# Performance work log

Measured on AMD Instinct MI355X. Metric: run time of the kernel, lower is better.

The kernel has to match this reference:

```python
import jax, jax.numpy as jnp
import numpy as np

T, B, E, H = 2048, 2, 1024, 16
DH = E // H
SCALE = DH ** -0.5
NEG = jnp.finfo(jnp.float32).min


def setup_inputs() -> dict:
    key = jax.random.key(0)
    ks = jax.random.split(key, 10)
    s = 0.02
    query = jax.random.normal(ks[0], (T, B, E), dtype=jnp.float32)
    key_padding_mask = jax.random.randint(ks[1], (B, T), 0, 2).astype(bool)
    # causal additive mask, broadcastable over (bsz, heads, tgt, src)
    causal = jnp.triu(jnp.ones((T, T), dtype=bool), k=1)
    attn_mask = jnp.where(causal, NEG, 0.0).astype(jnp.float32)[None, None]
    Wq = jax.random.normal(ks[2], (E, E), jnp.float32) * s
    bq = jax.random.normal(ks[3], (E,), jnp.float32) * s
    Wk = jax.random.normal(ks[4], (E, E), jnp.float32) * s
    bk = jax.random.normal(ks[5], (E,), jnp.float32) * s
    Wv = jax.random.normal(ks[6], (E, E), jnp.float32) * s
    bv = jax.random.normal(ks[7], (E,), jnp.float32) * s
    Wo = jax.random.normal(ks[8], (E, E), jnp.float32) * s
    bo = jax.random.normal(ks[9], (E,), jnp.float32) * s
    return {"query": query, "key_padding_mask": key_padding_mask, "attn_mask": attn_mask,
            "Wq": Wq, "bq": bq, "Wk": Wk, "bk": bk, "Wv": Wv, "bv": bv, "Wo": Wo, "bo": bo}


def _heads(x):
    # [T, B, E] -> [B, H, T, DH]
    return x.reshape(T, B, H, DH).transpose(1, 2, 0, 3)


def reference(query, key_padding_mask, attn_mask, Wq, bq, Wk, bk, Wv, bv, Wo, bo):
    # projections (torch Linear: x @ W.T + b); q scaled as in module
    q = _heads((query @ Wq.T + bq) * SCALE)          # [B,H,T,DH]
    k = _heads(query @ Wk.T + bk)                    # [B,H,S,DH] (self-attn: S=T)
    v = _heads(query @ Wv.T + bv)
    scores = jnp.einsum('bhtd,bhsd->bhts', q, k)     # [B,H,T,S]
    scores = scores + attn_mask                      # additive causal mask
    # key_padding_mask True -> masked_fill with dtype min
    scores = jnp.where(key_padding_mask[:, None, None, :], NEG, scores)
    probs = jax.nn.softmax(scores, axis=-1)
    ctx = jnp.einsum('bhts,bhsd->bhtd', probs, v)    # [B,H,T,DH]
    ctx = ctx.transpose(2, 0, 1, 3).reshape(T, B, E) # back to [T,B,E]
    return ctx @ Wo.T + bo
```

## Files before the change

### kernel.cpp

```cpp
#include <hip/hip_runtime.h>
#include <hip/hip_bf16.h>
#include <stdint.h>

typedef unsigned short u16;
typedef uint32_t u32;
typedef unsigned long long u64;
typedef __attribute__((ext_vector_type(8))) short bf16x8;
typedef __attribute__((ext_vector_type(4))) float f32x4;
typedef __attribute__((ext_vector_type(16))) float f32x16;
typedef __attribute__((ext_vector_type(4))) u32 u32x4;

#define T_SEQ 2048

__device__ __forceinline__ float bf2f(u16 u) {
  union { u32 i; float f; } v; v.i = ((u32)u) << 16; return v.f;
}
__device__ __forceinline__ u16 f2bf(float f) {
  union { float f; u32 i; } v; v.f = f;
  u32 u = v.i;
  return (u16)((u + 0x7fffu + ((u >> 16) & 1u)) >> 16);
}

#if __has_builtin(__builtin_amdgcn_exp2f)
#define EXP2F(x) __builtin_amdgcn_exp2f(x)
#else
#define EXP2F(x) exp2f(x)
#endif

__device__ __forceinline__ u32 permpack(float lo, float hi) {
#if __has_builtin(__builtin_amdgcn_perm)
  return __builtin_amdgcn_perm(__float_as_uint(hi), __float_as_uint(lo), 0x07060302u);
#else
  return (__float_as_uint(hi) & 0xFFFF0000u) | (__float_as_uint(lo) >> 16);
#endif
}

__device__ __forceinline__ void gload_lds16(const void* g, void* l) {
  __builtin_amdgcn_global_load_lds(
      (const __attribute__((address_space(1))) void*)g,
      (__attribute__((address_space(3))) void*)l, 16, 0, 0);
}

__global__ __launch_bounds__(256) void cvt_kernel(const float* __restrict__ src,
                                                  u16* __restrict__ dst, int n) {
  int i = (blockIdx.x * 256 + threadIdx.x) * 4;
  if (i + 3 < n) {
    const float4 v = *(const float4*)(src + i);
    ushort4 o;
    o.x = f2bf(v.x); o.y = f2bf(v.y); o.z = f2bf(v.z); o.w = f2bf(v.w);
    *(ushort4*)(dst + i) = o;
  }
}

__global__ __launch_bounds__(256) void cvt4_kernel(
    const float* __restrict__ s0, const float* __restrict__ s1,
    const float* __restrict__ s2, const float* __restrict__ s3,
    u16* __restrict__ dst) {
  const int z = blockIdx.y;
  const float* src = (z == 0) ? s0 : (z == 1) ? s1 : (z == 2) ? s2 : s3;
  int i = (blockIdx.x * 256 + threadIdx.x) * 4;
  const float4 v = *(const float4*)(src + i);
  ushort4 o;
  o.x = f2bf(v.x); o.y = f2bf(v.y); o.z = f2bf(v.z); o.w = f2bf(v.w);
  *(ushort4*)(dst + (size_t)z * 1048576 + i) = o;
}

__device__ __forceinline__ void gemm_core_128x128(
    f32x4 acc[2][4], const u16* __restrict__ A, const u16* __restrict__ Bw,
    int bm, int bn, u16* As, u16* Bs)
{
  const int tid = threadIdx.x;
  const int w = tid >> 6, lane = tid & 63, g = lane >> 4, c = lane & 15;
  const int wr = (w & 3) * 32, wc = (w >> 2) * 64;
  for (int k0 = 0; k0 < 1024; k0 += 64) {
    __syncthreads();
    #pragma unroll
    for (int is = 0; is < 2; ++is) {
      int o = (is*8 + w)*1024 + lane*16;
      int row = o >> 7, c16 = (o >> 4) & 7;
      gload_lds16(A + (size_t)(bm*128 + row)*1024 + k0 + (c16 ^ (row & 7))*8,
                  (char*)As + (is*8 + w)*1024);
    }
    #pragma unroll
    for (int is = 0; is < 2; ++is) {
      int o = (is*8 + w)*1024 + lane*16;
      int row = o >> 7, c16 = (o >> 4) & 7;
      gload_lds16(Bw + (size_t)(bn*128 + row)*1024 + k0 + (c16 ^ (row & 7))*8,
                  (char*)Bs + (is*8 + w)*1024);
    }
    __syncthreads();
    bf16x8 af[2][2], bfr[4][2];
    #pragma unroll
    for (int mf = 0; mf < 2; ++mf)
      #pragma unroll
      for (int kc = 0; kc < 2; ++kc) {
        int row = wr + mf*16 + c;
        int colb = kc*64 + g*16;
        af[mf][kc] = *(const bf16x8*)((const char*)As + row*128 + (colb ^ ((row & 7) << 4)));
      }
    #pragma unroll
    for (int nf = 0; nf < 4; ++nf)
      #pragma unroll
      for (int kc = 0; kc < 2; ++kc) {
        int row = wc + nf*16 + c;
        int colb = kc*64 + g*16;
        bfr[nf][kc] = *(const bf16x8*)((const char*)Bs + row*128 + (colb ^ ((row & 7) << 4)));
      }
    #pragma unroll
    for (int mf = 0; mf < 2; ++mf)
      #pragma unroll
      for (int nf = 0; nf < 4; ++nf)
        #pragma unroll
        for (int kc = 0; kc < 2; ++kc)
          acc[mf][nf] = __builtin_amdgcn_mfma_f32_16x16x32_bf16(
              af[mf][kc], bfr[nf][kc], acc[mf][nf], 0, 0, 0);
  }
}

__global__ __launch_bounds__(512, 2) void gemm_qkv(
    const u16* __restrict__ Abf, const u16* __restrict__ Wbf,
    const float* __restrict__ bq, const float* __restrict__ bk,
    const float* __restrict__ bv, u16* __restrict__ qkvh)
{
  __shared__ __align__(16) u16 As[128*64];
  __shared__ __align__(16) u16 Bs[128*64];
  f32x4 acc[2][4];
  #pragma unroll
  for (int mf = 0; mf < 2; ++mf)
    #pragma unroll
    for (int nf = 0; nf < 4; ++nf) acc[mf][nf] = (f32x4){0.f,0.f,0.f,0.f};
  gemm_core_128x128(acc, Abf, Wbf, blockIdx.x, blockIdx.y, As, Bs);
  const int tid = threadIdx.x, w = tid >> 6, lane = tid & 63, g = lane >> 4, c = lane & 15;
  const int wr = (w & 3) * 32, wc = (w >> 2) * 64;
  #pragma unroll
  for (int mf = 0; mf < 2; ++mf)
    #pragma unroll
    for (int nf = 0; nf < 4; ++nf) {
      int col = blockIdx.y*128 + wc + nf*16 + c;
      int z = col >> 10, colz = col & 1023;
      const float* bias = (z == 0) ? bq : (z == 1) ? bk : bv;
      float bcol = bias[colz];
      float scl = (z == 0) ? 0.18033688011112043f : 1.0f;
      int h = colz >> 6, d = colz & 63;
      u16* dst = qkvh + (size_t)z * 4194304;
      #pragma unroll
      for (int r = 0; r < 4; ++r) {
        int row = blockIdx.x*128 + wr + mf*16 + g*4 + r;
        int t = row >> 1, bb = row & 1;
        float v = (acc[mf][nf][r] + bcol) * scl;
        dst[(size_t)(bb*16 + h)*131072 + (size_t)t*64 + d] = f2bf(v);
      }
    }
}

__global__ __launch_bounds__(512, 2) void gemm_out(
    const u16* __restrict__ ctx2, const u16* __restrict__ Wobf,
    const float* __restrict__ bo, float* __restrict__ out)
{
  __shared__ __align__(16) u16 As[128*64];
  __shared__ __align__(16) u16 Bs[128*64];
  f32x4 acc[2][4];
  #pragma unroll
  for (int mf = 0; mf < 2; ++mf)
    #pragma unroll
    for (int nf = 0; nf < 4; ++nf) acc[mf][nf] = (f32x4){0.f,0.f,0.f,0.f};
  gemm_core_128x128(acc, ctx2, Wobf, blockIdx.x, blockIdx.y, As, Bs);
  const int tid = threadIdx.x, w = tid >> 6, lane = tid & 63, g = lane >> 4, c = lane & 15;
  const int wr = (w & 3) * 32, wc = (w >> 2) * 64;
  #pragma unroll
  for (int mf = 0; mf < 2; ++mf)
    #pragma unroll
    for (int nf = 0; nf < 4; ++nf) {
      int col = blockIdx.y*128 + wc + nf*16 + c;
      float bcol = bo[col];
      #pragma unroll
      for (int r = 0; r < 4; ++r) {
        int row = blockIdx.x*128 + wr + mf*16 + g*4 + r;
        out[(size_t)row*1024 + col] = acc[mf][nf][r] + bcol;
      }
    }
}

__global__ __launch_bounds__(256) void vtrans_kernel(const u16* __restrict__ Vh,
                                                     u16* __restrict__ Vt,
                                                     float* __restrict__ vs) {
  __shared__ u16 tile[64][72];
  const int bh = blockIdx.x >> 5, tc = blockIdx.x & 31;
  const int t0 = tc * 64;
  const int tid = threadIdx.x;
  {
    const int tl = tid >> 2, d0 = (tid & 3) * 16;
    const u16* src = Vh + (size_t)bh*131072 + (size_t)(t0 + tl)*64 + d0;
    bf16x8 a = *(const bf16x8*)src;
    bf16x8 b2 = *(const bf16x8*)(src + 8);
    #pragma unroll
    for (int j = 0; j < 8; ++j) {
      tile[d0 + j][tl] = (u16)a[j];
      tile[d0 + 8 + j][tl] = (u16)b2[j];
    }
  }
  __syncthreads();
  {
    const int d = tid >> 2, tq = (tid & 3) * 16;
    bf16x8 o0, o1;
    float s = 0.f;
    #pragma unroll
    for (int j = 0; j < 8; ++j) {
      u16 x0 = tile[d][tq + j], x1 = tile[d][tq + 8 + j];
      o0[j] = (short)x0; o1[j] = (short)x1;
      s += bf2f(x0) + bf2f(x1);
    }
    u16* dst = Vt + (size_t)bh*131072 + (size_t)d*2048 + t0 + tq;
    *(bf16x8*)dst = o0;
    *(bf16x8*)(dst + 8) = o1;
    s += __shfl_xor(s, 1, 64);
    s += __shfl_xor(s, 2, 64);
    if ((tid & 3) == 0) atomicAdd(&vs[bh*64 + d], s);
  }
}

#define ZERO16 (f32x16){0.f,0.f,0.f,0.f,0.f,0.f,0.f,0.f,0.f,0.f,0.f,0.f,0.f,0.f,0.f,0.f}
#define NEGINF (-__builtin_inff())

__global__ __launch_bounds__(128, 2) void flash_attn(
    const u16* __restrict__ Qh, const u16* __restrict__ Kh,
    const u16* __restrict__ Vt, const int* __restrict__ kpm,
    const float* __restrict__ vsum, u16* __restrict__ ctx2,
    u16* __restrict__ pctx, float* __restrict__ pml)
{
  __shared__ __align__(16) u16 Kl[2][4096];
  __shared__ __align__(16) u16 Vl[2][4096];

  const int tid = threadIdx.x;
  const int w = tid >> 6, lane = tid & 63;
  const int l31 = lane & 31, hi = lane >> 5;

  const int id = blockIdx.x;
  const int xcd = id & 7, rest = id >> 3;
  const int bh = xcd * 4 + (rest & 3);
  const int pr = rest >> 2;
  int k, ch, NS;
  if (pr < 32) { k = 31 - (pr >> 1); ch = pr & 1; NS = 2; }
  else         { k = 47 - pr;        ch = 0;      NS = 1; }
  const int nt = k + 1;
  const int b = bh >> 4, h = bh & 15;
  const size_t hbase = (size_t)bh * 131072;
  int lo, hicap;
  if (NS == 1) { lo = 0; hicap = nt; }
  else { int h1 = nt >> 1; lo = ch ? h1 : 0; hicap = ch ? nt : h1; }
  const int q = k*64 + w*32 + l31;

  bf16x8 qfrag[4];
  #pragma unroll
  for (int kt = 0; kt < 4; ++kt)
    qfrag[kt] = *(const bf16x8*)(Qh + hbase + (size_t)q*64 + kt*16 + hi*8);

  {
    const int s0t = lo * 64;
    if (w == 0) {
      #pragma unroll
      for (int is = 0; is < 8; ++is) {
        int o = is*1024 + lane*16;
        int row = o >> 7, c16 = (o >> 4) & 7;
        gload_lds16(Kh + hbase + (size_t)(s0t + row)*64 + (c16 ^ (row & 7))*8,
                    (char*)Kl[0] + is*1024);
      }
    } else {
      #pragma unroll
      for (int is = 0; is < 8; ++is) {
        int o = is*1024 + lane*16;
        int row = o >> 7, c16 = (o >> 4) & 7;
        gload_lds16(Vt + hbase + (size_t)row*2048 + s0t + (c16 ^ (row & 7))*8,
                    (char*)Vl[0] + is*1024);
      }
    }
  }
  int kpmv_cur = kpm[b*T_SEQ + lo*64 + lane];
  int kpmv_nxt = 0;
  __syncthreads();

  float mrow = NEGINF, lrow = 0.f;
  f32x16 cacc0 = ZERO16, cacc1 = ZERO16;

  for (int t = lo; t < hicap; ++t) {
    const int cur = (t - lo) & 1, nxt = cur ^ 1;
    const int s0 = t * 64;
    const bool notLast = (t + 1 < hicap);
    const bool diag = (t == nt - 1);

    if (notLast) {
      const int s0n = s0 + 64;
      if (w == 0) {
        #pragma unroll
        for (int is = 0; is < 8; ++is) {
          int o = is*1024 + lane*16;
          int row = o >> 7, c16 = (o >> 4) & 7;
          gload_lds16(Kh + hbase + (size_t)(s0n + row)*64 + (c16 ^ (row & 7))*8,
                      (char*)Kl[nxt] + is*1024);
        }
      } else {
        #pragma unroll
        for (int is = 0; is < 8; ++is) {
          int o = is*1024 + lane*16;
          int row = o >> 7, c16 = (o >> 4) & 7;
          gload_lds16(Vt + hbase + (size_t)row*2048 + s0n + (c16 ^ (row & 7))*8,
                      (char*)Vl[nxt] + is*1024);
        }
      }
      kpmv_nxt = kpm[b*T_SEQ + s0n + lane];
    }

    bf16x8 kreg[2][4], vf[2][4];
    #pragma unroll
    for (int sub = 0; sub < 2; ++sub)
      #pragma unroll
      for (int kt = 0; kt < 4; ++kt) {
        int row = sub*32 + l31;
        int colb = kt*32 + hi*16;
        kreg[sub][kt] = *(const bf16x8*)((const char*)Kl[cur] + row*128 + (colb ^ ((row & 7) << 4)));
        vf[sub][kt]   = *(const bf16x8*)((const char*)Vl[cur] + row*128 + (colb ^ ((row & 7) << 4)));
      }

    f32x16 st0 = ZERO16, st1 = ZERO16;
    __builtin_amdgcn_s_setprio(1);
    #pragma unroll
    for (int kt = 0; kt < 4; ++kt) {
      st0 = __builtin_amdgcn_mfma_f32_32x32x16_bf16(kreg[0][kt], qfrag[kt], st0, 0, 0, 0);
      st1 = __builtin_amdgcn_mfma_f32_32x32x16_bf16(kreg[1][kt], qfrag[kt], st1, 0, 0, 0);
    }
    __builtin_amdgcn_s_setprio(0);

    {
      const u64 mask = __ballot(kpmv_cur != 0);
      const u32 m0 = (u32)mask, m1 = (u32)(mask >> 32);
      const u64 m4 = mask >> 4;
      const u32 m4l = (u32)m4, m4h = (u32)(m4 >> 32);
      const u32 w0 = hi ? m4l : m0;
      const u32 w1 = hi ? m4h : m1;
      const int lim = q - s0 - 4*hi;
      #pragma unroll
      for (int m = 0; m < 4; ++m) {
        u32 nib0 = (w0 >> (m*8)) & 15u;
        u32 nib1 = (w1 >> (m*8)) & 15u;
        if (diag) {
          int t0c = lim - m*8;       int c0 = min(max(t0c + 1, 0), 4);
          int t1c = lim - 32 - m*8;  int c1 = min(max(t1c + 1, 0), 4);
          nib0 |= (0xFu << c0) & 0xFu;
          nib1 |= (0xFu << c1) & 0xFu;
        }
        #pragma unroll
        for (int r = 0; r < 4; ++r) {
          if ((nib0 >> r) & 1) st0[m*4 + r] = NEGINF;
          if ((nib1 >> r) & 1) st1[m*4 + r] = NEGINF;
        }
      }
      float t8[8];
      #pragma unroll
      for (int i = 0; i < 8; ++i)
        t8[i] = fmaxf(fmaxf(st0[i], st0[i+8]), fmaxf(st1[i], st1[i+8]));
      float t4a = fmaxf(t8[0], t8[4]), t4b = fmaxf(t8[1], t8[5]);
      float t4c = fmaxf(t8[2], t8[6]), t4d = fmaxf(t8[3], t8[7]);
      float rm = fmaxf(fmaxf(t4a, t4b), fmaxf(t4c, t4d));
      rm = fmaxf(rm, __shfl_xor(rm, 32, 64));

      const bool need = (rm > mrow + 8.f) || (mrow < -1e30f);
      if (__any(need)) {
        const float mn = fmaxf(mrow, rm);
        const float sc = (mn < -1e30f) ? 1.f : EXP2F(mrow - mn);
        mrow = mn;
        lrow *= sc;
        #pragma unroll
        for (int i = 0; i < 16; ++i) { cacc0[i] *= sc; cacc1[i] *= sc; }
      }
      const bool dead = (mrow < -1e30f);
      float a0 = 0.f, a1 = 0.f, a2 = 0.f, a3 = 0.f;
      #pragma unroll
      for (int i = 0; i < 16; i += 4) {
        float p0 = dead ? 0.f : EXP2F(st0[i+0] - mrow); st0[i+0] = p0; a0 += p0;
        float p1 = dead ? 0.f : EXP2F(st0[i+1] - mrow); st0[i+1] = p1; a1 += p1;
        float p2 = dead ? 0.f : EXP2F(st0[i+2] - mrow); st0[i+2] = p2; a2 += p2;
        float p3 = dead ? 0.f : EXP2F(st0[i+3] - mrow); st0[i+3] = p3; a3 += p3;
      }
      #pragma unroll
      for (int i = 0; i < 16; i += 4) {
        float p0 = dead ? 0.f : EXP2F(st1[i+0] - mrow); st1[i+0] = p0; a0 += p0;
        float p1 = dead ? 0.f : EXP2F(st1[i+1] - mrow); st1[i+1] = p1; a1 += p1;
        float p2 = dead ? 0.f : EXP2F(st1[i+2] - mrow); st1[i+2] = p2; a2 += p2;
        float p3 = dead ? 0.f : EXP2F(st1[i+3] - mrow); st1[i+3] = p3; a3 += p3;
      }
      float ps = (a0 + a1) + (a2 + a3);
      ps += __shfl_xor(ps, 32, 64);
      lrow += ps;
    }

    u32 pk[8][2];
    #pragma unroll
    for (int m = 0; m < 4; ++m) {
      pk[m][0]   = permpack(st0[m*4+0], st0[m*4+1]);
      pk[m][1]   = permpack(st0[m*4+2], st0[m*4+3]);
      pk[4+m][0] = permpack(st1[m*4+0], st1[m*4+1]);
      pk[4+m][1] = permpack(st1[m*4+2], st1[m*4+3]);
    }
    bf16x8 pf[4];
    #pragma unroll
    for (int ks = 0; ks < 4; ++ks) {
      u32 own0 = pk[2*ks][0],   own1 = pk[2*ks][1];
      u32 oth0 = pk[2*ks+1][0], oth1 = pk[2*ks+1][1];
      u32 r0 = __shfl_xor(hi ? own0 : oth0, 32, 64);
      u32 r1 = __shfl_xor(hi ? own1 : oth1, 32, 64);
      u32 w0 = hi ? r0 : own0;
      u32 w1 = hi ? r1 : own1;
      u32 w2 = hi ? oth0 : r0;
      u32 w3 = hi ? oth1 : r1;
      u32x4 wv = {w0, w1, w2, w3};
      pf[ks] = __builtin_bit_cast(bf16x8, wv);
    }

    __builtin_amdgcn_s_setprio(1);
    #pragma unroll
    for (int ks = 0; ks < 4; ++ks)
      cacc0 = __builtin_amdgcn_mfma_f32_32x32x16_bf16(vf[0][ks], pf[ks], cacc0, 0, 0, 0);
    #pragma unroll
    for (int ks = 0; ks < 4; ++ks)
      cacc1 = __builtin_amdgcn_mfma_f32_32x32x16_bf16(vf[1][ks], pf[ks], cacc1, 0, 0, 0);
    __builtin_amdgcn_s_setprio(0);

    kpmv_cur = kpmv_nxt;
    if (notLast) __syncthreads();
  }

  const int qt32 = 2*k + w;
  if (NS == 1) {
    const bool dead = (lrow == 0.f);
    const float rl = dead ? 0.f : 1.f / lrow;
    #pragma unroll
    for (int subd = 0; subd < 2; ++subd) {
      #pragma unroll
      for (int m = 0; m < 4; ++m) {
        const int d0 = subd*32 + hi*4 + m*8;
        float v0 = (subd ? cacc1[m*4+0] : cacc0[m*4+0]) * rl;
        float v1 = (subd ? cacc1[m*4+1] : cacc0[m*4+1]) * rl;
        float v2 = (subd ? cacc1[m*4+2] : cacc0[m*4+2]) * rl;
        float v3 = (subd ? cacc1[m*4+3] : cacc0[m*4+3]) * rl;
        if (dead) {
          const float* vs = vsum + bh*64 + d0;
          v0 = vs[0] * (1.0f/2048.0f);
          v1 = vs[1] * (1.0f/2048.0f);
          v2 = vs[2] * (1.0f/2048.0f);
          v3 = vs[3] * (1.0f/2048.0f);
        }
        ushort4 o;
        o.x = f2bf(v0); o.y = f2bf(v1); o.z = f2bf(v2); o.w = f2bf(v3);
        *(ushort4*)(ctx2 + (size_t)(q*2 + b)*1024 + h*64 + d0) = o;
      }
    }
  } else {
    const int slot = ((bh << 5) + (qt32 - 32))*2 + ch;
    u16* pc = pctx + (size_t)slot*2048 + (size_t)l31*64;
    #pragma unroll
    for (int subd = 0; subd < 2; ++subd) {
      #pragma unroll
      for (int m = 0; m < 4; ++m) {
        const int d0 = subd*32 + hi*4 + m*8;
        const f32x16& cc = subd ? cacc1 : cacc0;
        ushort4 o;
        o.x = f2bf(cc[m*4+0]); o.y = f2bf(cc[m*4+1]);
        o.z = f2bf(cc[m*4+2]); o.w = f2bf(cc[m*4+3]);
        *(ushort4*)(pc + d0) = o;
      }
    }
    if (!hi) {
      float2 ml; ml.x = mrow; ml.y = lrow;
      *(float2*)(pml + (size_t)slot*64 + l31*2) = ml;
    }
  }
}

__global__ __launch_bounds__(64) void combine_kernel(
    const u16* __restrict__ pctx, const float* __restrict__ pml,
    const float* __restrict__ vsum, u16* __restrict__ ctx2)
{
  const int qtm = blockIdx.x, bh = blockIdx.y;
  const int qt = 32 + qtm;
  const int b = bh >> 4, h = bh & 15;
  const int lane = threadIdx.x;
  const int qr = lane >> 1, d0 = (lane & 1) * 32;
  const int slot0 = ((bh << 5) + qtm)*2;
  const float* ml0 = pml + (size_t)slot0*64 + qr*2;
  const float* ml1 = pml + (size_t)(slot0+1)*64 + qr*2;
  const float m1 = ml0[0], l1 = ml0[1];
  const float m2 = ml1[0], l2 = ml1[1];
  const float ms = fmaxf(m1, m2);
  bool dead = (ms == NEGINF);
  const float w1 = dead ? 0.f : EXP2F(m1 - ms);
  const float w2 = dead ? 0.f : EXP2F(m2 - ms);
  const float lt = w1*l1 + w2*l2;
  dead = dead || (lt == 0.f);
  const float rl = dead ? 0.f : 1.f / lt;
  const u16* c1 = pctx + ((size_t)slot0*32 + qr)*64 + d0;
  const u16* c2 = pctx + ((size_t)(slot0+1)*32 + qr)*64 + d0;
  const int qrow = qt*32 + qr;
  u16* dst = ctx2 + (size_t)(qrow*2 + b)*1024 + h*64 + d0;
  #pragma unroll
  for (int g2 = 0; g2 < 4; ++g2) {
    bf16x8 a = *(const bf16x8*)(c1 + g2*8);
    bf16x8 bb = *(const bf16x8*)(c2 + g2*8);
    bf16x8 o;
    #pragma unroll
    for (int j = 0; j < 8; ++j) {
      float v = (w1*bf2f((u16)a[j]) + w2*bf2f((u16)bb[j])) * rl;
      if (dead) v = vsum[bh*64 + d0 + g2*8 + j] * (1.0f/2048.0f);
      o[j] = (short)f2bf(v);
    }
    *(bf16x8*)(dst + g2*8) = o;
  }
}

extern "C" void kernel_launch(void* const* d_in, const int* in_sizes, int n_in,
                              void* d_out, int out_size, void* d_ws, size_t ws_size,
                              hipStream_t stream) {
  const float* query = (const float*)d_in[0];
  const int*   kpm   = (const int*)d_in[1];
  const float* Wq = (const float*)d_in[3];
  const float* bq = (const float*)d_in[4];
  const float* Wk = (const float*)d_in[5];
  const float* bk = (const float*)d_in[6];
  const float* Wv = (const float*)d_in[7];
  const float* bv = (const float*)d_in[8];
  const float* Wo = (const float*)d_in[9];
  const float* bo = (const float*)d_in[10];

  char* ws = (char*)d_ws;
  u16*   qbf  = (u16*)(ws);
  u16*   Vt   = (u16*)(ws);
  u16*   wbf  = (u16*)(ws + 8388608);
  u16*   qkvh = (u16*)(ws + 16777216);
  u16*   pctx = (u16*)(ws + 33554432);
  u16*   ctx2 = (u16*)(ws + 41943040);
  float* vsum = (float*)(ws + 50331648);
  float* pml  = (float*)(ws + 50339840);

  cvt_kernel<<<dim3(4096), 256, 0, stream>>>(query, qbf, 4194304);
  cvt4_kernel<<<dim3(1024, 4), 256, 0, stream>>>(Wq, Wk, Wv, Wo, wbf);

  hipMemsetAsync(vsum, 0, 2048 * sizeof(float), stream);

  gemm_qkv<<<dim3(32, 24), 512, 0, stream>>>(qbf, wbf, bq, bk, bv, qkvh);
  vtrans_kernel<<<dim3(1024), 256, 0, stream>>>(qkvh + 2*4194304, Vt, vsum);
  flash_attn<<<dim3(1536), 128, 0, stream>>>(qkvh, qkvh + 1*4194304,
                                             Vt, kpm, vsum, ctx2, pctx, pml);
  combine_kernel<<<dim3(32, 32), 64, 0, stream>>>(pctx, pml, vsum, ctx2);
  gemm_out<<<dim3(32, 8), 512, 0, stream>>>(ctx2, wbf + 3*1048576, bo, (float*)d_out);
}
```

Before: 133.7 us.

## Widen flash attention blocks to 128 query rows and swizzle GEMM row tiles

Flash attention now runs 256-thread blocks that cover 128 query rows (4 waves) instead of 64. Each K/V tile loaded into shared memory is therefore reused by twice as many queries, and the K/V loads are split across all four waves. A packed lookup table assigns query tiles and split halves to blocks for load balance, and the partial-result slot layout and combine indexing are updated to match. The GEMM kernels also remap blockIdx.x across row tiles, apparently to spread or group M tiles across XCDs for better cache locality. The wider tile makes waves in one block process different causal extents, which risks idle waves on diagonal tiles and lower occupancy.

```diff
diff --git a/kernel.cpp b/kernel.cpp
--- a/kernel.cpp
+++ b/kernel.cpp
@@ -129,7 +129,9 @@
   for (int mf = 0; mf < 2; ++mf)
     #pragma unroll
     for (int nf = 0; nf < 4; ++nf) acc[mf][nf] = (f32x4){0.f,0.f,0.f,0.f};
-  gemm_core_128x128(acc, Abf, Wbf, blockIdx.x, blockIdx.y, As, Bs);
+  const int bx = blockIdx.x;
+  const int bm = (bx & 7) * 4 + (bx >> 3);
+  gemm_core_128x128(acc, Abf, Wbf, bm, blockIdx.y, As, Bs);
   const int tid = threadIdx.x, w = tid >> 6, lane = tid & 63, g = lane >> 4, c = lane & 15;
   const int wr = (w & 3) * 32, wc = (w >> 2) * 64;
   #pragma unroll
@@ -145,7 +147,7 @@
       u16* dst = qkvh + (size_t)z * 4194304;
       #pragma unroll
       for (int r = 0; r < 4; ++r) {
-        int row = blockIdx.x*128 + wr + mf*16 + g*4 + r;
+        int row = bm*128 + wr + mf*16 + g*4 + r;
         int t = row >> 1, bb = row & 1;
         float v = (acc[mf][nf][r] + bcol) * scl;
         dst[(size_t)(bb*16 + h)*131072 + (size_t)t*64 + d] = f2bf(v);
@@ -164,7 +166,9 @@
   for (int mf = 0; mf < 2; ++mf)
     #pragma unroll
     for (int nf = 0; nf < 4; ++nf) acc[mf][nf] = (f32x4){0.f,0.f,0.f,0.f};
-  gemm_core_128x128(acc, ctx2, Wobf, blockIdx.x, blockIdx.y, As, Bs);
+  const int bx = blockIdx.x;
+  const int bm = (bx & 7) * 4 + (bx >> 3);
+  gemm_core_128x128(acc, ctx2, Wobf, bm, blockIdx.y, As, Bs);
   const int tid = threadIdx.x, w = tid >> 6, lane = tid & 63, g = lane >> 4, c = lane & 15;
   const int wr = (w & 3) * 32, wc = (w >> 2) * 64;
   #pragma unroll
@@ -175,7 +179,7 @@
       float bcol = bo[col];
       #pragma unroll
       for (int r = 0; r < 4; ++r) {
-        int row = blockIdx.x*128 + wr + mf*16 + g*4 + r;
+        int row = bm*128 + wr + mf*16 + g*4 + r;
         out[(size_t)row*1024 + col] = acc[mf][nf][r] + bcol;
       }
     }
@@ -222,7 +226,7 @@
 #define ZERO16 (f32x16){0.f,0.f,0.f,0.f,0.f,0.f,0.f,0.f,0.f,0.f,0.f,0.f,0.f,0.f,0.f,0.f}
 #define NEGINF (-__builtin_inff())
 
-__global__ __launch_bounds__(128, 2) void flash_attn(
+__global__ __launch_bounds__(256, 2) void flash_attn(
     const u16* __restrict__ Qh, const u16* __restrict__ Kh,
     const u16* __restrict__ Vt, const int* __restrict__ kpm,
     const float* __restrict__ vsum, u16* __restrict__ ctx2,
@@ -239,16 +243,20 @@
   const int xcd = id & 7, rest = id >> 3;
   const int bh = xcd * 4 + (rest & 3);
   const int pr = rest >> 2;
-  int k, ch, NS;
-  if (pr < 32) { k = 31 - (pr >> 1); ch = pr & 1; NS = 2; }
-  else         { k = 47 - pr;        ch = 0;      NS = 1; }
-  const int nt = k + 1;
+  const u64 k0t = 0x9AA5BBCC6DDEE7FFULL, k1t = 0x94883210ULL;
+  const u64 m0t = 0x0102101021010210ULL, m1t = 0x12102222ULL;
+  const int k  = (int)(((pr < 16) ? (k0t >> (pr*4)) : (k1t >> ((pr-16)*4))) & 15);
+  const int md = (int)(((pr < 16) ? (m0t >> (pr*4)) : (m1t >> ((pr-16)*4))) & 3);
+  const int NS = (md == 2) ? 1 : 2, ch = md & 1;
+
+  const int ntmax = 2*k + 2;
   const int b = bh >> 4, h = bh & 15;
   const size_t hbase = (size_t)bh * 131072;
   int lo, hicap;
-  if (NS == 1) { lo = 0; hicap = nt; }
-  else { int h1 = nt >> 1; lo = ch ? h1 : 0; hicap = ch ? nt : h1; }
-  const int q = k*64 + w*32 + l31;
+  if (NS == 1) { lo = 0; hicap = ntmax; }
+  else { lo = ch ? (k+1) : 0; hicap = ch ? ntmax : (k+1); }
+  const int q = 128*k + 32*w + l31;
+  const int myNt = 2*k + 1 + (w >> 1);
 
   bf16x8 qfrag[4];
   #pragma unroll
@@ -257,21 +265,22 @@
 
   {
     const int s0t = lo * 64;
-    if (w == 0) {
-      #pragma unroll
-      for (int is = 0; is < 8; ++is) {
-        int o = is*1024 + lane*16;
+    const int jb = (w & 1) * 4;
+    if (w < 2) {
+      #pragma unroll
+      for (int is = 0; is < 4; ++is) {
+        int o = (jb + is)*1024 + lane*16;
         int row = o >> 7, c16 = (o >> 4) & 7;
         gload_lds16(Kh + hbase + (size_t)(s0t + row)*64 + (c16 ^ (row & 7))*8,
-                    (char*)Kl[0] + is*1024);
+                    (char*)Kl[0] + (jb + is)*1024);
       }
     } else {
       #pragma unroll
-      for (int is = 0; is < 8; ++is) {
-        int o = is*1024 + lane*16;
+      for (int is = 0; is < 4; ++is) {
+        int o = (jb + is)*1024 + lane*16;
         int row = o >> 7, c16 = (o >> 4) & 7;
         gload_lds16(Vt + hbase + (size_t)row*2048 + s0t + (c16 ^ (row & 7))*8,
-                    (char*)Vl[0] + is*1024);
+                    (char*)Vl[0] + (jb + is)*1024);
       }
     }
   }
@@ -286,25 +295,26 @@
     const int cur = (t - lo) & 1, nxt = cur ^ 1;
     const int s0 = t * 64;
     const bool notLast = (t + 1 < hicap);
-    const bool diag = (t == nt - 1);
+    const bool diag = (t >= myNt - 1);
 
     if (notLast) {
       const int s0n = s0 + 64;
-      if (w == 0) {
+      const int jb = (w & 1) * 4;
+      if (w < 2) {
         #pragma unroll
-        for (int is = 0; is < 8; ++is) {
-          int o = is*1024 + lane*16;
+        for (int is = 0; is < 4; ++is) {
+          int o = (jb + is)*1024 + lane*16;
           int row = o >> 7, c16 = (o >> 4) & 7;
           gload_lds16(Kh + hbase + (size_t)(s0n + row)*64 + (c16 ^ (row & 7))*8,
-                      (char*)Kl[nxt] + is*1024);
+                      (char*)Kl[nxt] + (jb + is)*1024);
         }
       } else {
         #pragma unroll
-        for (int is = 0; is < 8; ++is) {
-          int o = is*1024 + lane*16;
+        for (int is = 0; is < 4; ++is) {
+          int o = (jb + is)*1024 + lane*16;
           int row = o >> 7, c16 = (o >> 4) & 7;
           gload_lds16(Vt + hbase + (size_t)row*2048 + s0n + (c16 ^ (row & 7))*8,
-                      (char*)Vl[nxt] + is*1024);
+                      (char*)Vl[nxt] + (jb + is)*1024);
         }
       }
       kpmv_nxt = kpm[b*T_SEQ + s0n + lane];
@@ -429,7 +439,6 @@
     if (notLast) __syncthreads();
   }
 
-  const int qt32 = 2*k + w;
   if (NS == 1) {
     const bool dead = (lrow == 0.f);
     const float rl = dead ? 0.f : 1.f / lrow;
@@ -455,8 +464,9 @@
       }
     }
   } else {
-    const int slot = ((bh << 5) + (qt32 - 32))*2 + ch;
-    u16* pc = pctx + (size_t)slot*2048 + (size_t)l31*64;
+    const int slot = ((bh << 3) + (k - 8))*2 + ch;
+    const int row = w*32 + l31;
+    u16* pc = pctx + ((size_t)slot*128 + row)*64;
     #pragma unroll
     for (int subd = 0; subd < 2; ++subd) {
       #pragma unroll
@@ -471,7 +481,7 @@
     }
     if (!hi) {
       float2 ml; ml.x = mrow; ml.y = lrow;
-      *(float2*)(pml + (size_t)slot*64 + l31*2) = ml;
+      *(float2*)(pml + ((size_t)slot*128 + row)*2) = ml;
     }
   }
 }
@@ -482,12 +492,14 @@
 {
   const int qtm = blockIdx.x, bh = blockIdx.y;
   const int qt = 32 + qtm;
+  const int k = qt >> 2, wq = qt & 3;
   const int b = bh >> 4, h = bh & 15;
   const int lane = threadIdx.x;
   const int qr = lane >> 1, d0 = (lane & 1) * 32;
-  const int slot0 = ((bh << 5) + qtm)*2;
-  const float* ml0 = pml + (size_t)slot0*64 + qr*2;
-  const float* ml1 = pml + (size_t)(slot0+1)*64 + qr*2;
+  const int slot0 = ((bh << 3) + (k - 8))*2;
+  const int row = wq*32 + qr;
+  const float* ml0 = pml + ((size_t)slot0*128 + row)*2;
+  const float* ml1 = pml + ((size_t)(slot0+1)*128 + row)*2;
   const float m1 = ml0[0], l1 = ml0[1];
   const float m2 = ml1[0], l2 = ml1[1];
   const float ms = fmaxf(m1, m2);
@@ -497,8 +509,8 @@
   const float lt = w1*l1 + w2*l2;
   dead = dead || (lt == 0.f);
   const float rl = dead ? 0.f : 1.f / lt;
-  const u16* c1 = pctx + ((size_t)slot0*32 + qr)*64 + d0;
-  const u16* c2 = pctx + ((size_t)(slot0+1)*32 + qr)*64 + d0;
+  const u16* c1 = pctx + ((size_t)slot0*128 + row)*64 + d0;
+  const u16* c2 = pctx + ((size_t)(slot0+1)*128 + row)*64 + d0;
   const int qrow = qt*32 + qr;
   u16* dst = ctx2 + (size_t)(qrow*2 + b)*1024 + h*64 + d0;
   #pragma unroll
@@ -547,8 +559,8 @@
 
   gemm_qkv<<<dim3(32, 24), 512, 0, stream>>>(qbf, wbf, bq, bk, bv, qkvh);
   vtrans_kernel<<<dim3(1024), 256, 0, stream>>>(qkvh + 2*4194304, Vt, vsum);
-  flash_attn<<<dim3(1536), 128, 0, stream>>>(qkvh, qkvh + 1*4194304,
-                                             Vt, kpm, vsum, ctx2, pctx, pml);
+  flash_attn<<<dim3(768), 256, 0, stream>>>(qkvh, qkvh + 1*4194304,
+                                            Vt, kpm, vsum, ctx2, pctx, pml);
   combine_kernel<<<dim3(32, 32), 64, 0, stream>>>(pctx, pml, vsum, ctx2);
   gemm_out<<<dim3(32, 8), 512, 0, stream>>>(ctx2, wbf + 3*1048576, bo, (float*)d_out);
 }
```

Result: no change. 134.4 us (+0.5%).
